# Optimization experiments

Hardware: AMD Instinct MI355X
Metric: run time of the kernel (lower is better)

## Reference

```python
import jax, jax.numpy as jnp
import numpy as np

B, N, D, H = 4, 1024, 768, 12
DH = D // H
HIDDEN = 4 * D
EPS = 1e-6


def _layernorm(x, g, b):
    mu = jnp.mean(x, axis=-1, keepdims=True)
    var = jnp.mean(jnp.square(x - mu), axis=-1, keepdims=True)
    return (x - mu) * jax.lax.rsqrt(var + EPS) * g + b


def setup_inputs() -> dict:
    key = jax.random.key(0)
    ks = jax.random.split(key, 8)
    s = 0.02  # init scale for weights
    return {
        "x": jax.random.normal(ks[0], (B, N, D), jnp.float32),
        "adj_bias": jax.random.normal(ks[1], (N, N), jnp.float32) * 0.1,
        "ln1_g": jnp.ones((D,), jnp.float32),
        "ln1_b": jnp.zeros((D,), jnp.float32),
        "qkv_w": jax.random.normal(ks[2], (D, 3 * D), jnp.float32) * s,
        "qkv_b": jnp.zeros((3 * D,), jnp.float32),
        "proj_w": jax.random.normal(ks[3], (D, D), jnp.float32) * s,
        "proj_b": jnp.zeros((D,), jnp.float32),
        "ln2_g": jnp.ones((D,), jnp.float32),
        "ln2_b": jnp.zeros((D,), jnp.float32),
        "fc1_w": jax.random.normal(ks[4], (D, HIDDEN), jnp.float32) * s,
        "fc1_b": jnp.zeros((HIDDEN,), jnp.float32),
        "fc2_w": jax.random.normal(ks[5], (HIDDEN, D), jnp.float32) * s,
        "fc2_b": jnp.zeros((D,), jnp.float32),
    }


def reference(x, adj_bias, ln1_g, ln1_b, qkv_w, qkv_b, proj_w, proj_b,
              ln2_g, ln2_b, fc1_w, fc1_b, fc2_w, fc2_b):
    scale = DH ** -0.5
    # --- attention with additive adjacency bias ---
    h = _layernorm(x, ln1_g, ln1_b)
    qkv = (h @ qkv_w + qkv_b).reshape(B, N, 3, H, DH)
    q, k, v = (jnp.moveaxis(qkv, 2, 0)[i].transpose(0, 2, 1, 3) for i in range(3))  # [B,H,N,DH]
    scores = jnp.einsum('bhqd,bhkd->bhqk', q, k) * scale + adj_bias[None, None]
    w = jax.nn.softmax(scores, axis=-1)
    attn = jnp.einsum('bhqk,bhkd->bhqd', w, v)          # [B,H,N,DH]
    attn = attn.transpose(0, 2, 1, 3).reshape(B, N, D)  # [B,N,D]
    x = x + (attn @ proj_w + proj_b)
    # --- MLP ---
    h2 = _layernorm(x, ln2_g, ln2_b)
    m = jax.nn.gelu(h2 @ fc1_w + fc1_b, approximate=False) @ fc2_w + fc2_b
    return x + m
```

## Files before the change

### kernel.cpp

```cpp
#include <hip/hip_runtime.h>
#include <cstdint>
#include <cstring>

typedef unsigned short u16;
typedef __attribute__((ext_vector_type(8))) short short8;
typedef __attribute__((ext_vector_type(4))) float float4v;

#define BB 4
#define NN 1024
#define DD 768
#define HH 12
#define DHH 64
#define HID 3072
#define MM (BB*NN)

__device__ __forceinline__ u16 f2b(float f) {
  unsigned int u = __float_as_uint(f);
  u += 0x7FFF + ((u >> 16) & 1);
  return (u16)(u >> 16);
}
__device__ __forceinline__ float b2f(u16 h) {
  return __uint_as_float(((unsigned int)h) << 16);
}

__device__ __forceinline__ void gll16(const void* g, void* l) {
  __builtin_amdgcn_global_load_lds(
      (const __attribute__((address_space(1))) unsigned int*)g,
      (__attribute__((address_space(3))) unsigned int*)l, 16, 0, 0);
}

__global__ __launch_bounds__(256)
void prep_k(const float* __restrict__ qkvw, const float* __restrict__ projw,
            const float* __restrict__ fc1w, const float* __restrict__ fc2w,
            const float* __restrict__ adj,
            u16* __restrict__ wtqkv, u16* __restrict__ wtproj,
            u16* __restrict__ wtfc1, u16* __restrict__ wtfc2,
            u16* __restrict__ adjP) {
  __shared__ float tile[32][33];
  const int id = blockIdx.x, t = threadIdx.x;
  if (id < 6912) {
    const float* w; u16* wt; int K, N, tid;
    if (id < 1728)      { w = qkvw;  wt = wtqkv;  K = DD;  N = 3 * DD; tid = id; }
    else if (id < 2304) { w = projw; wt = wtproj; K = DD;  N = DD;     tid = id - 1728; }
    else if (id < 4608) { w = fc1w;  wt = wtfc1;  K = DD;  N = HID;    tid = id - 2304; }
    else                { w = fc2w;  wt = wtfc2;  K = HID; N = DD;     tid = id - 4608; }
    const int ntiles = N / 32;
    const int n0 = (tid % ntiles) * 32, k0 = (tid / ntiles) * 32;
    const int tx = t & 31, ty = t >> 5;
#pragma unroll
    for (int i = 0; i < 4; i++)
      tile[ty + i * 8][tx] = w[(size_t)(k0 + ty + i * 8) * N + n0 + tx];
    __syncthreads();
#pragma unroll
    for (int i = 0; i < 4; i++)
      wt[(size_t)(n0 + ty + i * 8) * K + k0 + tx] = f2b(tile[tx][ty + i * 8]);
  } else {
    const int aid = id - 6912;
    const int qt = aid >> 4, kt = aid & 15;
    const int wv = t >> 6, q4 = (t >> 4) & 3, m15 = t & 15;
    u16 v[16];
#pragma unroll
    for (int ct = 0; ct < 4; ct++)
#pragma unroll
      for (int r = 0; r < 4; r++)
        v[ct * 4 + r] =
            f2b(adj[(size_t)(qt * 64 + wv * 16 + q4 * 4 + r) * NN + kt * 64 + ct * 16 + m15]);
    u16* dst = adjP + (size_t)aid * 4096 + t * 16;
    *(uint4*)dst = *(const uint4*)&v[0];
    *(uint4*)(dst + 8) = *(const uint4*)&v[8];
  }
}

__global__ __launch_bounds__(256)
void ln_k(const float* __restrict__ x, const float* __restrict__ g,
          const float* __restrict__ b, u16* __restrict__ o) {
  const int row = blockIdx.x, t = threadIdx.x;
  const float* xr = x + (size_t)row * DD;
  float v0 = xr[t], v1 = xr[t + 256], v2 = xr[t + 512];
  float s = v0 + v1 + v2;
  float s2 = v0 * v0 + v1 * v1 + v2 * v2;
#pragma unroll
  for (int off = 32; off > 0; off >>= 1) {
    s += __shfl_down(s, off);
    s2 += __shfl_down(s2, off);
  }
  __shared__ float rs[4], rs2[4], bc[2];
  const int lane = t & 63, wv = t >> 6;
  if (lane == 0) { rs[wv] = s; rs2[wv] = s2; }
  __syncthreads();
  if (t == 0) {
    float ts = rs[0] + rs[1] + rs[2] + rs[3];
    float ts2 = rs2[0] + rs2[1] + rs2[2] + rs2[3];
    float mean = ts * (1.f / DD);
    float var = ts2 * (1.f / DD) - mean * mean;
    bc[0] = mean;
    bc[1] = rsqrtf(var + 1e-6f);
  }
  __syncthreads();
  const float mean = bc[0], rstd = bc[1];
  u16* orow = o + (size_t)row * DD;
  orow[t]       = f2b((v0 - mean) * rstd * g[t]       + b[t]);
  orow[t + 256] = f2b((v1 - mean) * rstd * g[t + 256] + b[t + 256]);
  orow[t + 512] = f2b((v2 - mean) * rstd * g[t + 512] + b[t + 512]);
}

template <int MODE, int TN, int BK, int NC>
__global__ __launch_bounds__(256, 4)
void gemm_k(const u16* __restrict__ A, const u16* __restrict__ Bt,
            const float* __restrict__ bias, const float* __restrict__ resid,
            float* __restrict__ outf, u16* __restrict__ outb,
            u16* __restrict__ outq, u16* __restrict__ outk, u16* __restrict__ outv,
            int K) {
  __shared__ u16 As[2][128 * BK];
  __shared__ u16 Bs[2][TN * BK];
  constexpr int JM = TN / 32;
  constexpr int KK = BK / 32;
  constexpr int SLOTS = BK / 8;
  constexpr int AI = BK / 4;
  constexpr int BI = TN * BK / 512;
  constexpr int VC = (AI + BI) / 4;
  constexpr int NB = NC / TN;
  constexpr int RN = NB / 2;

  const int id = blockIdx.x;
  const int xcd = id & 7, idx = id >> 3;
  const int tileN = ((xcd & 1) * RN + idx % RN) * TN;
  const int tileM = ((xcd >> 1) * 8 + idx / RN) * 128;

  const int lane = threadIdx.x & 63, wave = threadIdx.x >> 6;
  const int wrow = (wave >> 1) * 64, wcol = (wave & 1) * (TN / 2);
  const int m15 = lane & 15, q4 = lane >> 4;
  const int rkey = (BK == 32) ? ((m15 >> 1) & 3) : (m15 & 7);

  float4v acc[4][JM];
#pragma unroll
  for (int i = 0; i < 4; i++)
#pragma unroll
    for (int j = 0; j < JM; j++) acc[i][j] = (float4v)0.f;

  auto stage = [&](int kt, int buf) {
    const int kk0 = kt * BK;
#pragma unroll
    for (int q = wave; q < AI; q += 4) {
      const int c = q * 64 + lane;
      const int row = c / SLOTS, slot = c % SLOTS;
      const int key = (BK == 32) ? ((row >> 1) & 3) : (row & 7);
      gll16(A + (size_t)(tileM + row) * K + kk0 + (slot ^ key) * 8, &As[buf][q * 512]);
    }
#pragma unroll
    for (int q = wave; q < BI; q += 4) {
      const int c = q * 64 + lane;
      const int row = c / SLOTS, slot = c % SLOTS;
      const int key = (BK == 32) ? ((row >> 1) & 3) : (row & 7);
      gll16(Bt + (size_t)(tileN + row) * K + kk0 + (slot ^ key) * 8, &Bs[buf][q * 512]);
    }
  };

  const int T = K / BK;
  stage(0, 0);
  for (int kt = 0; kt < T; ++kt) {
    const int cur = kt & 1;
    if (kt + 1 < T) {
      stage(kt + 1, cur ^ 1);
      asm volatile("s_waitcnt vmcnt(%0)\n\ts_barrier" :: "n"(VC) : "memory");
    } else {
      asm volatile("s_waitcnt vmcnt(0)\n\ts_barrier" ::: "memory");
    }
    short8 af[4][KK], bfr[JM][KK];
#pragma unroll
    for (int i = 0; i < 4; i++)
#pragma unroll
      for (int kk = 0; kk < KK; kk++)
        af[i][kk] = *(const short8*)(
            &As[cur][(wrow + i * 16 + m15) * BK + (((kk * 4 + q4) ^ rkey)) * 8]);
#pragma unroll
    for (int j = 0; j < JM; j++)
#pragma unroll
      for (int kk = 0; kk < KK; kk++)
        bfr[j][kk] = *(const short8*)(
            &Bs[cur][(wcol + j * 16 + m15) * BK + (((kk * 4 + q4) ^ rkey)) * 8]);
#pragma unroll
    for (int i = 0; i < 4; i++)
#pragma unroll
      for (int j = 0; j < JM; j++)
#pragma unroll
        for (int kk = 0; kk < KK; kk++)
          acc[i][j] =
              __builtin_amdgcn_mfma_f32_16x16x32_bf16(af[i][kk], bfr[j][kk], acc[i][j], 0, 0, 0);
    asm volatile("s_waitcnt lgkmcnt(0)\n\ts_barrier" ::: "memory");
  }

#pragma unroll
  for (int i = 0; i < 4; i++) {
#pragma unroll
    for (int j = 0; j < JM; j++) {
      const int col = tileN + wcol + j * 16 + m15;
#pragma unroll
      for (int r = 0; r < 4; r++) {
        const int row = tileM + wrow + i * 16 + q4 * 4 + r;
        float v = acc[i][j][r] + bias[col];
        if (MODE == 1) {
          outf[(size_t)row * NC + col] = resid[(size_t)row * NC + col] + v;
        } else if (MODE == 2) {
          float gv = 0.5f * v * (1.f + erff(v * 0.70710678f));
          outb[(size_t)row * NC + col] = f2b(gv);
        } else {
          const int three = col / DD, hh = (col % DD) >> 6, dh = col & 63;
          const int bb = row >> 10, nn = row & 1023;
          if (three == 2) {
            outv[(((size_t)(bb * HH + hh)) * DHH + dh) * NN + nn] = f2b(v);
          } else {
            const size_t idx2 = (((size_t)(bb * HH + hh)) * NN + nn) * DHH + dh;
            (three == 0 ? outq : outk)[idx2] = f2b(v);
          }
        }
      }
    }
  }
}

__global__ __launch_bounds__(256, 4)
void attn_k(const u16* __restrict__ qw, const u16* __restrict__ kw,
            const u16* __restrict__ vtw, const u16* __restrict__ adjP,
            u16* __restrict__ out) {
  __shared__ u16 Ks[64][72];
  __shared__ u16 Vt[64][72];
  __shared__ u16 Pb[4][16][72];

  const int id = blockIdx.x;
  const int bh = (id & 7) * 6 + ((id >> 3) >> 4);
  const int qt = (id >> 3) & 15;
  const int t = threadIdx.x, lane = t & 63, wave = t >> 6;
  const int m15 = lane & 15, q4 = lane >> 4;

  const u16* qrow = qw + ((size_t)bh * NN + qt * 64 + wave * 16 + m15) * DHH;
  const short8 qf0 = *(const short8*)(qrow + q4 * 8);
  const short8 qf1 = *(const short8*)(qrow + 32 + q4 * 8);

  float lreg[4] = {0.f, 0.f, 0.f, 0.f};
  float4v o[4];
#pragma unroll
  for (int ct = 0; ct < 4; ct++) o[ct] = (float4v)0.f;

  const u16* kbase0 = kw + (size_t)bh * NN * DHH;
  const u16* vtbase0 = vtw + (size_t)bh * DHH * NN;
  const u16* abase = adjP + (size_t)qt * 16 * 4096 + t * 16;

  const int r0 = t >> 3;
  const int c80 = (t & 7) * 8;

  uint4 kr0 = *(const uint4*)(kbase0 + r0 * 64 + c80);
  uint4 kr1 = *(const uint4*)(kbase0 + (r0 + 32) * 64 + c80);
  uint4 vr0 = *(const uint4*)(vtbase0 + (size_t)r0 * NN + c80);
  uint4 vr1 = *(const uint4*)(vtbase0 + (size_t)(r0 + 32) * NN + c80);

  for (int kt = 0; kt < 16; kt++) {
    __syncthreads();
    *(uint4*)&Ks[r0][c80] = kr0;
    *(uint4*)&Ks[r0 + 32][c80] = kr1;
    *(uint4*)&Vt[r0][c80] = vr0;
    *(uint4*)&Vt[r0 + 32][c80] = vr1;
    __syncthreads();
    if (kt < 15) {
      const u16* kb = kbase0 + (size_t)(kt + 1) * 64 * DHH;
      const u16* vb = vtbase0 + (kt + 1) * 64;
      kr0 = *(const uint4*)(kb + r0 * 64 + c80);
      kr1 = *(const uint4*)(kb + (r0 + 32) * 64 + c80);
      vr0 = *(const uint4*)(vb + (size_t)r0 * NN + c80);
      vr1 = *(const uint4*)(vb + (size_t)(r0 + 32) * NN + c80);
    }
    u16 av[16];
    const u16* ap = abase + (size_t)kt * 4096;
    *(uint4*)&av[0] = *(const uint4*)ap;
    *(uint4*)&av[8] = *(const uint4*)(ap + 8);

    float4v s[4];
#pragma unroll
    for (int ct = 0; ct < 4; ct++) s[ct] = (float4v)0.f;
#pragma unroll
    for (int ct = 0; ct < 4; ct++) {
      short8 b = *(const short8*)&Ks[ct * 16 + m15][q4 * 8];
      s[ct] = __builtin_amdgcn_mfma_f32_16x16x32_bf16(qf0, b, s[ct], 0, 0, 0);
    }
#pragma unroll
    for (int ct = 0; ct < 4; ct++) {
      short8 b = *(const short8*)&Ks[ct * 16 + m15][32 + q4 * 8];
      s[ct] = __builtin_amdgcn_mfma_f32_16x16x32_bf16(qf1, b, s[ct], 0, 0, 0);
    }

#pragma unroll
    for (int ct = 0; ct < 4; ct++)
#pragma unroll
      for (int r = 0; r < 4; r++) {
        float v = s[ct][r] * 0.125f + b2f(av[ct * 4 + r]);
        u16 pb = f2b(__expf(v));
        Pb[wave][q4 * 4 + r][ct * 16 + m15] = pb;
        lreg[r] += b2f(pb);
      }

    asm volatile("s_waitcnt lgkmcnt(0)" ::: "memory");

    short8 a0 = *(const short8*)&Pb[wave][m15][q4 * 8];
    short8 a1 = *(const short8*)&Pb[wave][m15][32 + q4 * 8];
#pragma unroll
    for (int ct = 0; ct < 4; ct++) {
      short8 b = *(const short8*)&Vt[ct * 16 + m15][q4 * 8];
      o[ct] = __builtin_amdgcn_mfma_f32_16x16x32_bf16(a0, b, o[ct], 0, 0, 0);
    }
#pragma unroll
    for (int ct = 0; ct < 4; ct++) {
      short8 b = *(const short8*)&Vt[ct * 16 + m15][32 + q4 * 8];
      o[ct] = __builtin_amdgcn_mfma_f32_16x16x32_bf16(a1, b, o[ct], 0, 0, 0);
    }
  }

#pragma unroll
  for (int off = 1; off < 16; off <<= 1)
#pragma unroll
    for (int r = 0; r < 4; r++) lreg[r] += __shfl_xor(lreg[r], off);

  const int bb2 = bh / HH, hh = bh % HH;
  const int row0 = qt * 64 + wave * 16 + q4 * 4;
#pragma unroll
  for (int ct = 0; ct < 4; ct++)
#pragma unroll
    for (int r = 0; r < 4; r++)
      out[((size_t)(bb2 * NN + row0 + r)) * DD + hh * 64 + ct * 16 + m15] =
          f2b(o[ct][r] / lreg[r]);
}

extern "C" void kernel_launch(void* const* d_in, const int* in_sizes, int n_in,
                              void* d_out, int out_size, void* d_ws, size_t ws_size,
                              hipStream_t stream) {
  const float* x     = (const float*)d_in[0];
  const float* adj   = (const float*)d_in[1];
  const float* ln1g  = (const float*)d_in[2];
  const float* ln1b  = (const float*)d_in[3];
  const float* qkvw  = (const float*)d_in[4];
  const float* qkvb  = (const float*)d_in[5];
  const float* projw = (const float*)d_in[6];
  const float* projb = (const float*)d_in[7];
  const float* ln2g  = (const float*)d_in[8];
  const float* ln2b  = (const float*)d_in[9];
  const float* fc1w  = (const float*)d_in[10];
  const float* fc1b  = (const float*)d_in[11];
  const float* fc2w  = (const float*)d_in[12];
  const float* fc2b  = (const float*)d_in[13];
  float* out = (float*)d_out;

  char* ws = (char*)d_ws;
  u16* wtqkv = (u16*)ws;  ws += (size_t)DD * (3 * DD) * 2;
  u16* wtproj = (u16*)ws; ws += (size_t)DD * DD * 2;
  u16* wtfc1 = (u16*)ws;  ws += (size_t)DD * HID * 2;
  u16* wtfc2 = (u16*)ws;  ws += (size_t)HID * DD * 2;
  u16* adjP = (u16*)ws;   ws += (size_t)NN * NN * 2;
  u16* hbuf = (u16*)ws;   ws += (size_t)MM * DD * 2;
  u16* qws = (u16*)ws;    ws += (size_t)MM * DD * 2;
  u16* kws = (u16*)ws;    ws += (size_t)MM * DD * 2;
  u16* vtws = (u16*)ws;   ws += (size_t)MM * DD * 2;
  u16* attnb = (u16*)ws;  ws += (size_t)MM * DD * 2;
  u16* h2buf = (u16*)ws;  ws += (size_t)MM * DD * 2;
  u16* a1buf = (u16*)ws;  ws += (size_t)MM * HID * 2;

  prep_k<<<7168, 256, 0, stream>>>(qkvw, projw, fc1w, fc2w, adj,
                                   wtqkv, wtproj, wtfc1, wtfc2, adjP);

  ln_k<<<MM, 256, 0, stream>>>(x, ln1g, ln1b, hbuf);

  gemm_k<0, 128, 32, 3 * DD><<<((3 * DD) / 128) * (MM / 128), 256, 0, stream>>>(
      hbuf, wtqkv, qkvb, nullptr, nullptr, nullptr, qws, kws, vtws, DD);

  attn_k<<<(NN / 64) * (BB * HH), 256, 0, stream>>>(qws, kws, vtws, adjP, attnb);

  gemm_k<1, 64, 64, DD><<<(DD / 64) * (MM / 128), 256, 0, stream>>>(
      attnb, wtproj, projb, x, out, nullptr, nullptr, nullptr, nullptr, DD);

  ln_k<<<MM, 256, 0, stream>>>(out, ln2g, ln2b, h2buf);

  gemm_k<2, 128, 32, HID><<<(HID / 128) * (MM / 128), 256, 0, stream>>>(
      h2buf, wtfc1, fc1b, nullptr, nullptr, a1buf, nullptr, nullptr, nullptr, DD);

  gemm_k<1, 64, 64, DD><<<(DD / 64) * (MM / 128), 256, 0, stream>>>(
      a1buf, wtfc2, fc2b, out, out, nullptr, nullptr, nullptr, nullptr, HID);
}
```

Measured before the change: 284.9 us.

## Triple-buffer GEMM LDS tiles and make K a compile-time parameter

Result: slower. 416.0 us (+46.0%).

```diff
diff --git a/kernel.cpp b/kernel.cpp
--- a/kernel.cpp
+++ b/kernel.cpp
@@ -104,15 +104,14 @@
   orow[t + 512] = f2b((v2 - mean) * rstd * g[t + 512] + b[t + 512]);
 }
 
-template <int MODE, int TN, int BK, int NC>
-__global__ __launch_bounds__(256, 4)
+template <int MODE, int TN, int BK, int KD, int NC>
+__global__ __launch_bounds__(256, (TN == 128) ? 3 : 2)
 void gemm_k(const u16* __restrict__ A, const u16* __restrict__ Bt,
             const float* __restrict__ bias, const float* __restrict__ resid,
             float* __restrict__ outf, u16* __restrict__ outb,
-            u16* __restrict__ outq, u16* __restrict__ outk, u16* __restrict__ outv,
-            int K) {
-  __shared__ u16 As[2][128 * BK];
-  __shared__ u16 Bs[2][TN * BK];
+            u16* __restrict__ outq, u16* __restrict__ outk, u16* __restrict__ outv) {
+  __shared__ u16 As[3][128 * BK];
+  __shared__ u16 Bs[3][TN * BK];
   constexpr int JM = TN / 32;
   constexpr int KK = BK / 32;
   constexpr int SLOTS = BK / 8;
@@ -121,6 +120,7 @@
   constexpr int VC = (AI + BI) / 4;
   constexpr int NB = NC / TN;
   constexpr int RN = NB / 2;
+  constexpr int T = KD / BK;
 
   const int id = blockIdx.x;
   const int xcd = id & 7, idx = id >> 3;
@@ -145,40 +145,31 @@
       const int c = q * 64 + lane;
       const int row = c / SLOTS, slot = c % SLOTS;
       const int key = (BK == 32) ? ((row >> 1) & 3) : (row & 7);
-      gll16(A + (size_t)(tileM + row) * K + kk0 + (slot ^ key) * 8, &As[buf][q * 512]);
+      gll16(A + (size_t)(tileM + row) * KD + kk0 + (slot ^ key) * 8, &As[buf][q * 512]);
     }
 #pragma unroll
     for (int q = wave; q < BI; q += 4) {
       const int c = q * 64 + lane;
       const int row = c / SLOTS, slot = c % SLOTS;
       const int key = (BK == 32) ? ((row >> 1) & 3) : (row & 7);
-      gll16(Bt + (size_t)(tileN + row) * K + kk0 + (slot ^ key) * 8, &Bs[buf][q * 512]);
+      gll16(Bt + (size_t)(tileN + row) * KD + kk0 + (slot ^ key) * 8, &Bs[buf][q * 512]);
     }
   };
 
-  const int T = K / BK;
-  stage(0, 0);
-  for (int kt = 0; kt < T; ++kt) {
-    const int cur = kt & 1;
-    if (kt + 1 < T) {
-      stage(kt + 1, cur ^ 1);
-      asm volatile("s_waitcnt vmcnt(%0)\n\ts_barrier" :: "n"(VC) : "memory");
-    } else {
-      asm volatile("s_waitcnt vmcnt(0)\n\ts_barrier" ::: "memory");
-    }
+  auto compute = [&](int buf) {
     short8 af[4][KK], bfr[JM][KK];
 #pragma unroll
     for (int i = 0; i < 4; i++)
 #pragma unroll
       for (int kk = 0; kk < KK; kk++)
         af[i][kk] = *(const short8*)(
-            &As[cur][(wrow + i * 16 + m15) * BK + (((kk * 4 + q4) ^ rkey)) * 8]);
+            &As[buf][(wrow + i * 16 + m15) * BK + (((kk * 4 + q4) ^ rkey)) * 8]);
 #pragma unroll
     for (int j = 0; j < JM; j++)
 #pragma unroll
       for (int kk = 0; kk < KK; kk++)
         bfr[j][kk] = *(const short8*)(
-            &Bs[cur][(wcol + j * 16 + m15) * BK + (((kk * 4 + q4) ^ rkey)) * 8]);
+            &Bs[buf][(wcol + j * 16 + m15) * BK + (((kk * 4 + q4) ^ rkey)) * 8]);
 #pragma unroll
     for (int i = 0; i < 4; i++)
 #pragma unroll
@@ -187,8 +178,18 @@
         for (int kk = 0; kk < KK; kk++)
           acc[i][j] =
               __builtin_amdgcn_mfma_f32_16x16x32_bf16(af[i][kk], bfr[j][kk], acc[i][j], 0, 0, 0);
-    asm volatile("s_waitcnt lgkmcnt(0)\n\ts_barrier" ::: "memory");
-  }
+  };
+
+  stage(0, 0);
+  stage(1, 1);
+#pragma unroll
+  for (int kt = 0; kt < T - 1; ++kt) {
+    asm volatile("s_waitcnt vmcnt(%0)\n\ts_barrier" :: "n"(VC) : "memory");
+    if (kt + 2 < T) stage(kt + 2, (kt + 2) % 3);
+    compute(kt % 3);
+  }
+  asm volatile("s_waitcnt vmcnt(0)\n\ts_barrier" ::: "memory");
+  compute((T - 1) % 3);
 
 #pragma unroll
   for (int i = 0; i < 4; i++) {
@@ -367,19 +368,19 @@
 
   ln_k<<<MM, 256, 0, stream>>>(x, ln1g, ln1b, hbuf);
 
-  gemm_k<0, 128, 32, 3 * DD><<<((3 * DD) / 128) * (MM / 128), 256, 0, stream>>>(
-      hbuf, wtqkv, qkvb, nullptr, nullptr, nullptr, qws, kws, vtws, DD);
+  gemm_k<0, 128, 32, DD, 3 * DD><<<((3 * DD) / 128) * (MM / 128), 256, 0, stream>>>(
+      hbuf, wtqkv, qkvb, nullptr, nullptr, nullptr, qws, kws, vtws);
 
   attn_k<<<(NN / 64) * (BB * HH), 256, 0, stream>>>(qws, kws, vtws, adjP, attnb);
 
-  gemm_k<1, 64, 64, DD><<<(DD / 64) * (MM / 128), 256, 0, stream>>>(
-      attnb, wtproj, projb, x, out, nullptr, nullptr, nullptr, nullptr, DD);
+  gemm_k<1, 64, 64, DD, DD><<<(DD / 64) * (MM / 128), 256, 0, stream>>>(
+      attnb, wtproj, projb, x, out, nullptr, nullptr, nullptr, nullptr);
 
   ln_k<<<MM, 256, 0, stream>>>(out, ln2g, ln2b, h2buf);
 
-  gemm_k<2, 128, 32, HID><<<(HID / 128) * (MM / 128), 256, 0, stream>>>(
-      h2buf, wtfc1, fc1b, nullptr, nullptr, a1buf, nullptr, nullptr, nullptr, DD);
-
-  gemm_k<1, 64, 64, DD><<<(DD / 64) * (MM / 128), 256, 0, stream>>>(
-      a1buf, wtfc2, fc2b, out, out, nullptr, nullptr, nullptr, nullptr, HID);
-}
+  gemm_k<2, 128, 32, DD, HID><<<(HID / 128) * (MM / 128), 256, 0, stream>>>(
+      h2buf, wtfc1, fc1b, nullptr, nullptr, a1buf, nullptr, nullptr, nullptr);
+
+  gemm_k<1, 64, 64, HID, DD><<<(DD / 64) * (MM / 128), 256, 0, stream>>>(
+      a1buf, wtfc2, fc2b, out, out, nullptr, nullptr, nullptr, nullptr);
+}
```
